# Kernel optimization log

Measured on AMD Instinct MI355X. Metric: run time of the kernel, lower is better.

## Reference

```python
import jax, jax.numpy as jnp
import numpy as np

NUM_HEADS = 16
NUM_KV_HEADS = 4
HEAD_DIM = 128
ROPE_DIMS = 64
EPS = 1.1920929e-07  # torch.finfo(float32).eps, used by F.rms_norm(eps=None)


def rms_norm(x):
    ms = jnp.mean(jnp.square(x), axis=-1, keepdims=True)
    return x * jax.lax.rsqrt(ms + EPS)


def apply_rotary(x, cos, sin):
    # x: [..., s, rope_dims]; cos/sin: [s, rope_dims//2]
    h = x.shape[-1] // 2
    x1, x2 = x[..., :h], x[..., h:]
    return jnp.concatenate([x1 * cos + x2 * sin, -x1 * sin + x2 * cos], axis=-1)


def setup_inputs() -> dict:
    key = jax.random.key(0)
    ks = jax.random.split(key, 5)
    b, s, d = 2, 2048, 2048
    return {
        "x": jax.random.normal(ks[0], (b, s, d), jnp.float32),
        "q_w": jax.random.normal(ks[1], (d, d), jnp.float32) * 0.02,
        "k_w": jax.random.normal(ks[2], (NUM_KV_HEADS * HEAD_DIM, d), jnp.float32) * 0.02,
        "v_w": jax.random.normal(ks[3], (NUM_KV_HEADS * HEAD_DIM, d), jnp.float32) * 0.02,
        "out_w": jax.random.normal(ks[4], (d, d), jnp.float32) * 0.02,
        "q_gain": jnp.full((NUM_HEADS,), 12.0, jnp.float32),
    }


def reference(x, q_w, k_w, v_w, out_w, q_gain):
    b, s, d = x.shape
    g = NUM_HEADS // NUM_KV_HEADS

    q = (x @ q_w.T).reshape(b, s, NUM_HEADS, HEAD_DIM).transpose(0, 2, 1, 3)
    k = (x @ k_w.T).reshape(b, s, NUM_KV_HEADS, HEAD_DIM).transpose(0, 2, 1, 3)
    v = (x @ v_w.T).reshape(b, s, NUM_KV_HEADS, HEAD_DIM).transpose(0, 2, 1, 3)

    q = rms_norm(q)
    k = rms_norm(k)

    # partial rotary embedding
    t = jnp.arange(s, dtype=jnp.float32)
    inv_freq = 1.0 / (10000.0 ** (jnp.arange(0, ROPE_DIMS, 2, dtype=jnp.float32) / ROPE_DIMS))
    f = jnp.outer(t, inv_freq)                      # [s, rope_dims//2]
    cos, sin = jnp.cos(f), jnp.sin(f)

    q = jnp.concatenate([apply_rotary(q[..., :ROPE_DIMS], cos, sin), q[..., ROPE_DIMS:]], axis=-1)
    q = q * q_gain[None, :, None, None]
    k = jnp.concatenate([apply_rotary(k[..., :ROPE_DIMS], cos, sin), k[..., ROPE_DIMS:]], axis=-1)

    # GQA-native causal attention (no repeated K/V materialization)
    qg = q.reshape(b, NUM_KV_HEADS, g, s, HEAD_DIM)
    scale = 1.0 / jnp.sqrt(jnp.float32(HEAD_DIM))
    scores = jnp.einsum("bkgqd,bkld->bkgql", qg, k) * scale
    causal = jnp.tril(jnp.ones((s, s), bool))
    scores = jnp.where(causal, scores, jnp.finfo(scores.dtype).min)
    p = jax.nn.softmax(scores, axis=-1)
    y = jnp.einsum("bkgql,bkld->bkgqd", p, v)       # [b, kvh, g, s, hd]
    y = y.reshape(b, NUM_HEADS, s, HEAD_DIM).transpose(0, 2, 1, 3).reshape(b, s, d)
    return y @ out_w.T
```

## Files before the change

### kernel.cpp

```cpp
#include <hip/hip_runtime.h>
#include <cmath>


#define S_LEN 2048
#define DMODEL 2048
#define NH 16
#define NKV 4
#define HD 128

#define NEG_SENT -1.0e30f
#define QK_SCALE 0.08838834764831845f

typedef _Float16 f16x8 __attribute__((ext_vector_type(8)));
typedef float f32x4 __attribute__((ext_vector_type(4)));

static __device__ __forceinline__ short f2h(float f) {
  _Float16 h = (_Float16)f;
  return *(short*)&h;
}
static __device__ __forceinline__ float h2f(short s) {
  _Float16 h = *(_Float16*)&s;
  return (float)h;
}

static __device__ __forceinline__ void stage16(const short* g, short* ldsbase) {
  __builtin_amdgcn_global_load_lds(
      (const __attribute__((address_space(1))) void*)g,
      (__attribute__((address_space(3))) void*)ldsbase, 16, 0, 0);
}

__global__ __launch_bounds__(256) void f32_to_f16(const float* __restrict__ src,
                                                  short* __restrict__ dst, int n) {
  int i = (blockIdx.x * 256 + threadIdx.x) * 4;
  if (i < n) {
    float4 v = *reinterpret_cast<const float4*>(src + i);
    short4 o;
    o.x = f2h(v.x); o.y = f2h(v.y); o.z = f2h(v.z); o.w = f2h(v.w);
    *reinterpret_cast<short4*>(dst + i) = o;
  }
}

template <bool F32OUT>
static __device__ __forceinline__ void gemm_core(const short* __restrict__ A,
                                                 const short* __restrict__ W,
                                                 void* __restrict__ Cv,
                                                 int N, int K, int bm, int bn) {
  __shared__ __align__(16) short As[128][64];
  __shared__ __align__(16) short Ws[128][64];
  const int tid = threadIdx.x;
  const int wave = tid >> 6, lane = tid & 63;
  const int quad = lane >> 4, l16 = lane & 15;
  const int wm = (wave >> 1) * 64, wn = (wave & 1) * 64;

  f32x4 acc[4][4];
#pragma unroll
  for (int i = 0; i < 4; i++)
#pragma unroll
    for (int j = 0; j < 4; j++) acc[i][j] = f32x4{0.f, 0.f, 0.f, 0.f};

  const int srow = wave * 8 + (lane >> 3);
  const int scol = (lane & 7) * 8;

  for (int k0 = 0; k0 < K; k0 += 64) {
    __syncthreads();
#pragma unroll
    for (int i = 0; i < 4; i++) {
      stage16(A + (size_t)(bm + srow + i * 32) * K + k0 + scol,
              &As[wave * 8 + i * 32][0]);
      stage16(W + (size_t)(bn + srow + i * 32) * K + k0 + scol,
              &Ws[wave * 8 + i * 32][0]);
    }
    __syncthreads();
#pragma unroll
    for (int kk = 0; kk < 64; kk += 32) {
      f16x8 af[4], bfr[4];
#pragma unroll
      for (int mi = 0; mi < 4; mi++)
        af[mi] = *reinterpret_cast<const f16x8*>(&As[wm + mi * 16 + l16][kk + quad * 8]);
#pragma unroll
      for (int ni = 0; ni < 4; ni++)
        bfr[ni] = *reinterpret_cast<const f16x8*>(&Ws[wn + ni * 16 + l16][kk + quad * 8]);
#pragma unroll
      for (int mi = 0; mi < 4; mi++)
#pragma unroll
        for (int ni = 0; ni < 4; ni++)
          acc[mi][ni] = __builtin_amdgcn_mfma_f32_16x16x32_f16(af[mi], bfr[ni], acc[mi][ni], 0, 0, 0);
    }
  }
#pragma unroll
  for (int mi = 0; mi < 4; mi++)
#pragma unroll
    for (int ni = 0; ni < 4; ni++) {
      int gr = bm + wm + mi * 16 + quad * 4;
      int gc = bn + wn + ni * 16 + l16;
#pragma unroll
      for (int r = 0; r < 4; r++) {
        if (F32OUT)
          ((float*)Cv)[(size_t)(gr + r) * N + gc] = acc[mi][ni][r];
        else
          ((short*)Cv)[(size_t)(gr + r) * N + gc] = f2h(acc[mi][ni][r]);
      }
    }
}

template <bool F32OUT>
__global__ __launch_bounds__(256) void gemm_bt(const short* __restrict__ A,
                                               const short* __restrict__ W,
                                               void* __restrict__ Cv,
                                               int N, int K) {
  gemm_core<F32OUT>(A, W, Cv, N, K, blockIdx.x * 128, blockIdx.y * 128);
}

__global__ __launch_bounds__(256) void gemm_kv(const short* __restrict__ A,
                                               const short* __restrict__ W0,
                                               const short* __restrict__ W1,
                                               short* __restrict__ C0,
                                               short* __restrict__ C1,
                                               int N, int K) {
  const short* W = blockIdx.z ? W1 : W0;
  short* C = blockIdx.z ? C1 : C0;
  gemm_core<false>(A, W, (void*)C, N, K, blockIdx.x * 128, blockIdx.y * 128);
}

__global__ __launch_bounds__(256) void postproc(const short* __restrict__ src,
                                                short* __restrict__ dst,
                                                const float* __restrict__ gain,
                                                int n_heads, int mode) {
  int gw = blockIdx.x * 4 + (threadIdx.x >> 6);
  int lane = threadIdx.x & 63;
  int head = gw % n_heads;
  int token = gw / n_heads;
  int s = token & (S_LEN - 1);
  int b = token >> 11;
  const short* sp = src + (size_t)token * (n_heads * HD) + head * HD;
  float v0 = h2f(sp[lane]);
  float v1 = h2f(sp[lane + 64]);
  float ss = v0 * v0 + v1 * v1;
#pragma unroll
  for (int off = 1; off < 64; off <<= 1) ss += __shfl_xor(ss, off, 64);
  float sc = rsqrtf(ss * (1.0f / 128.0f) + 1.1920929e-07f);
  v0 *= sc;
  v1 *= sc;
  int i = lane & 31;
  float inv = powf(10000.0f, -((float)(2 * i) * (1.0f / 64.0f)));
  float f = (float)s * inv;
  float cs, sn;
  sincosf(f, &sn, &cs);
  float partner = __shfl_xor(v0, 32, 64);
  v0 = (lane < 32) ? (v0 * cs + partner * sn) : (v0 * cs - partner * sn);
  if (mode == 2) {
    float g = gain[head] * QK_SCALE;
    v0 *= g;
    v1 *= g;
  }
  short* dp = dst + ((size_t)(b * n_heads + head) * S_LEN + s) * HD;
  dp[lane] = f2h(v0);
  dp[lane + 64] = f2h(v1);
}

__global__ __launch_bounds__(256) void v_transpose(const short* __restrict__ src,
                                                   short* __restrict__ dst) {
  __shared__ __align__(16) short t[64][72];
  const int tid = threadIdx.x;
  const int s0 = blockIdx.x * 64;
  const int d0 = blockIdx.y * 64;
#pragma unroll
  for (int i = 0; i < 2; i++) {
    int r = (tid >> 3) + i * 32;
    int c = (tid & 7) * 8;
    *reinterpret_cast<int4*>(&t[r][c]) =
        *reinterpret_cast<const int4*>(src + (size_t)(s0 + r) * 512 + d0 + c);
  }
  __syncthreads();
  const int b = s0 >> 11;
  const int sbase = s0 & (S_LEN - 1);
#pragma unroll
  for (int i = 0; i < 2; i++) {
    int dr = (tid >> 3) + i * 32;
    int sc8 = (tid & 7) * 8;
    int d = d0 + dr;
    int kv = d >> 7, dw = d & 127;
    short4 lo, hi;
    lo.x = t[sc8 + 0][dr]; lo.y = t[sc8 + 1][dr];
    lo.z = t[sc8 + 2][dr]; lo.w = t[sc8 + 3][dr];
    hi.x = t[sc8 + 4][dr]; hi.y = t[sc8 + 5][dr];
    hi.z = t[sc8 + 6][dr]; hi.w = t[sc8 + 7][dr];
    short* dp = dst + (((size_t)(b * NKV + kv) * HD + dw) * S_LEN) + sbase + sc8;
    *reinterpret_cast<short4*>(dp) = lo;
    *reinterpret_cast<short4*>(dp + 4) = hi;
  }
}

__global__ __launch_bounds__(256, 2) void attn_fwd(const short* __restrict__ qb,
                                                   const short* __restrict__ kb,
                                                   const short* __restrict__ vT,
                                                   short* __restrict__ out) {
  __shared__ __align__(16) short k_lds[64][136];
  __shared__ __align__(16) short vt_lds[144][72];
  __shared__ __align__(16) short p_lds[4][16][136];

  const int tid = threadIdx.x, wave = tid >> 6, lane = tid & 63;
  const int quad = lane >> 4, l16 = lane & 15;
  const int bh = blockIdx.y;
  const int b = bh >> 4, h = bh & 15;
  const int kvh = h >> 2;
  const int pj = blockIdx.x;

  const short* kptr = kb + ((size_t)(b * NKV + kvh) * S_LEN) * HD;
  const short* vtp  = vT + ((size_t)(b * NKV + kvh) * HD) * S_LEN;

  const int kr = (tid >> 4), kc = (tid & 15) * 8;
  const int vr = (tid >> 3), vc = (tid & 7) * 8;

  {
    int r = 128 + (tid >> 4);
    int c = (tid & 15) * 4;
    short val = (r == 128) ? (short)0x3C00 : (short)0;
    short4 v4 = {val, val, val, val};
    *reinterpret_cast<short4*>(&vt_lds[r][c]) = v4;
  }

  for (int pass = 0; pass < 2; pass++) {
    const int qsub = pass ? (31 - pj) : pj;
    const int q0 = qsub * 64 + wave * 16;
    const short* qptr = qb + ((size_t)(b * NH + h) * S_LEN + q0) * HD;

    f16x8 qf[4];
#pragma unroll
    for (int st = 0; st < 4; st++)
      qf[st] = *reinterpret_cast<const f16x8*>(
          qptr + (size_t)l16 * HD + st * 32 + quad * 8);

    f32x4 o[9];
#pragma unroll
    for (int i = 0; i < 9; i++) o[i] = f32x4{0.f, 0.f, 0.f, 0.f};
    float m_i[4] = {NEG_SENT, NEG_SENT, NEG_SENT, NEG_SENT};

    const int ktiles = qsub + 1;
    for (int kt = 0; kt < ktiles; kt++) {
      const int kbase = kt * 64;
      __syncthreads();
#pragma unroll
      for (int i = 0; i < 4; i++)
        *reinterpret_cast<int4*>(&k_lds[kr + i * 16][kc]) =
            *reinterpret_cast<const int4*>(kptr + (size_t)(kbase + kr + i * 16) * HD + kc);
#pragma unroll
      for (int i = 0; i < 4; i++)
        *reinterpret_cast<int4*>(&vt_lds[vr + i * 32][vc]) =
            *reinterpret_cast<const int4*>(vtp + (size_t)(vr + i * 32) * S_LEN + kbase + vc);
      __syncthreads();

      f32x4 sc[4];
#pragma unroll
      for (int ct = 0; ct < 4; ct++) sc[ct] = f32x4{0.f, 0.f, 0.f, 0.f};
#pragma unroll
      for (int ct = 0; ct < 4; ct++) {
#pragma unroll
        for (int st = 0; st < 4; st++) {
          f16x8 kf = *reinterpret_cast<const f16x8*>(&k_lds[ct * 16 + l16][st * 32 + quad * 8]);
          sc[ct] = __builtin_amdgcn_mfma_f32_16x16x32_f16(qf[st], kf, sc[ct], 0, 0, 0);
        }
      }

      if (kbase + 63 > q0) {
#pragma unroll
        for (int ct = 0; ct < 4; ct++)
#pragma unroll
          for (int r = 0; r < 4; r++) {
            int qrow = q0 + quad * 4 + r;
            int col = kbase + ct * 16 + l16;
            sc[ct][r] = (col <= qrow) ? sc[ct][r] : NEG_SENT;
          }
      }

      float cand[4];
#pragma unroll
      for (int r = 0; r < 4; r++)
        cand[r] = fmaxf(fmaxf(sc[0][r], sc[1][r]), fmaxf(sc[2][r], sc[3][r]));
#pragma unroll
      for (int off = 1; off < 16; off <<= 1)
#pragma unroll
        for (int r = 0; r < 4; r++)
          cand[r] = fmaxf(cand[r], __shfl_xor(cand[r], off, 64));

      bool ch = (cand[0] > m_i[0]) | (cand[1] > m_i[1]) |
                (cand[2] > m_i[2]) | (cand[3] > m_i[3]);
      if (__any(ch)) {
        float alpha[4];
#pragma unroll
        for (int r = 0; r < 4; r++) {
          float mn = fmaxf(m_i[r], cand[r]);
          alpha[r] = __expf(m_i[r] - mn);
          m_i[r] = mn;
        }
#pragma unroll
        for (int nt = 0; nt < 9; nt++)
#pragma unroll
          for (int r = 0; r < 4; r++) o[nt][r] *= alpha[r];
      }

#pragma unroll
      for (int ct = 0; ct < 4; ct++)
#pragma unroll
        for (int r = 0; r < 4; r++) {
          float p = __expf(sc[ct][r] - m_i[r]);
          p_lds[wave][quad * 4 + r][ct * 16 + l16] = f2h(p);
        }

      f16x8 pf0 = *reinterpret_cast<const f16x8*>(&p_lds[wave][l16][quad * 8]);
      f16x8 pf1 = *reinterpret_cast<const f16x8*>(&p_lds[wave][l16][32 + quad * 8]);
#pragma unroll
      for (int nt = 0; nt < 9; nt++) {
        f16x8 vf0 = *reinterpret_cast<const f16x8*>(&vt_lds[nt * 16 + l16][quad * 8]);
        f16x8 vf1 = *reinterpret_cast<const f16x8*>(&vt_lds[nt * 16 + l16][32 + quad * 8]);
        o[nt] = __builtin_amdgcn_mfma_f32_16x16x32_f16(pf0, vf0, o[nt], 0, 0, 0);
        o[nt] = __builtin_amdgcn_mfma_f32_16x16x32_f16(pf1, vf1, o[nt], 0, 0, 0);
      }
    }

    float inv_l[4];
#pragma unroll
    for (int r = 0; r < 4; r++) {
      float l = __shfl(o[8][r], lane & 48, 64);
      inv_l[r] = 1.0f / fmaxf(l, 1e-20f);
    }
#pragma unroll
    for (int nt = 0; nt < 8; nt++)
#pragma unroll
      for (int r = 0; r < 4; r++) {
        int srow = q0 + quad * 4 + r;
        int dcol = nt * 16 + l16;
        out[((size_t)(b * S_LEN + srow)) * DMODEL + h * HD + dcol] =
            f2h(o[nt][r] * inv_l[r]);
      }
  }
}

extern "C" void kernel_launch(void* const* d_in, const int* in_sizes, int n_in,
                              void* d_out, int out_size, void* d_ws, size_t ws_size,
                              hipStream_t stream) {
  const float* x      = (const float*)d_in[0];
  const float* q_w    = (const float*)d_in[1];
  const float* k_w    = (const float*)d_in[2];
  const float* v_w    = (const float*)d_in[3];
  const float* out_w  = (const float*)d_in[4];
  const float* q_gain = (const float*)d_in[5];
  float* out = (float*)d_out;

  const int BS = 2 * S_LEN;
  short* xb   = (short*)d_ws;
  short* wqb  = xb   + (size_t)8 * 1024 * 1024;
  short* wkb  = wqb  + (size_t)4 * 1024 * 1024;
  short* wvb  = wkb  + (size_t)1 * 1024 * 1024;
  short* wob  = wvb  + (size_t)1 * 1024 * 1024;
  short* qraw = wob  + (size_t)4 * 1024 * 1024;
  short* kraw = qraw + (size_t)8 * 1024 * 1024;
  short* vraw = kraw + (size_t)2 * 1024 * 1024;
  short* qbuf = vraw + (size_t)2 * 1024 * 1024;
  short* kbuf = qbuf + (size_t)8 * 1024 * 1024;
  short* vT   = kbuf + (size_t)2 * 1024 * 1024;
  short* attn = qraw;

  dim3 blk(256);
  f32_to_f16<<<8192, blk, 0, stream>>>(x, xb, BS * DMODEL);
  f32_to_f16<<<4096, blk, 0, stream>>>(q_w, wqb, DMODEL * DMODEL);
  f32_to_f16<<<1024, blk, 0, stream>>>(k_w, wkb, 512 * DMODEL);
  f32_to_f16<<<1024, blk, 0, stream>>>(v_w, wvb, 512 * DMODEL);
  f32_to_f16<<<4096, blk, 0, stream>>>(out_w, wob, DMODEL * DMODEL);

  gemm_bt<false><<<dim3(32, 16), blk, 0, stream>>>(xb, wqb, qraw, 2048, 2048);
  gemm_kv<<<dim3(32, 4, 2), blk, 0, stream>>>(xb, wkb, wvb, kraw, vraw, 512, 2048);

  postproc<<<dim3((BS * NH) / 4), blk, 0, stream>>>(qraw, qbuf, q_gain, NH, 2);
  postproc<<<dim3((BS * NKV) / 4), blk, 0, stream>>>(kraw, kbuf, q_gain, NKV, 1);
  v_transpose<<<dim3(BS / 64, 8), blk, 0, stream>>>(vraw, vT);

  attn_fwd<<<dim3(16, 2 * NH), blk, 0, stream>>>(qbuf, kbuf, vT, attn);

  gemm_bt<true><<<dim3(32, 16), blk, 0, stream>>>(attn, wob, out, 2048, 2048);
}
```

Baseline: 387.7 us.

## Fuse fp32-to-fp16 casts, prefetch K/V tiles in registers, remap attention grid

Merges the five conversion launches into one kernel that picks its source buffer by global index. In attention, the next K/V tile is loaded into registers while the current tile is computed, so global latency overlaps with MFMA work. The launch becomes a 1D grid ordered so blocks sharing a KV head run close together, which should help L2 reuse. p_lds is also shrunk, freeing LDS, at the cost of extra register pressure from the prefetch buffers.

```diff
diff --git a/kernel.cpp b/kernel.cpp
--- a/kernel.cpp
+++ b/kernel.cpp
@@ -29,15 +29,31 @@
       (__attribute__((address_space(3))) void*)ldsbase, 16, 0, 0);
 }
 
-__global__ __launch_bounds__(256) void f32_to_f16(const float* __restrict__ src,
-                                                  short* __restrict__ dst, int n) {
-  int i = (blockIdx.x * 256 + threadIdx.x) * 4;
-  if (i < n) {
-    float4 v = *reinterpret_cast<const float4*>(src + i);
-    short4 o;
-    o.x = f2h(v.x); o.y = f2h(v.y); o.z = f2h(v.z); o.w = f2h(v.w);
-    *reinterpret_cast<short4*>(dst + i) = o;
-  }
+__global__ __launch_bounds__(256) void f32_to_f16_all(
+    const float* __restrict__ s0, const float* __restrict__ s1,
+    const float* __restrict__ s2, const float* __restrict__ s3,
+    const float* __restrict__ s4, short* __restrict__ d0,
+    short* __restrict__ d1, short* __restrict__ d2, short* __restrict__ d3,
+    short* __restrict__ d4) {
+  int u = blockIdx.x * 256 + threadIdx.x;
+  const float* src;
+  short* dst;
+  int off;
+  if (u < 2097152) {
+    src = s0; dst = d0; off = u;
+  } else if (u < 3145728) {
+    src = s1; dst = d1; off = u - 2097152;
+  } else if (u < 3407872) {
+    src = s2; dst = d2; off = u - 3145728;
+  } else if (u < 3670016) {
+    src = s3; dst = d3; off = u - 3407872;
+  } else {
+    src = s4; dst = d4; off = u - 3670016;
+  }
+  float4 v = *reinterpret_cast<const float4*>(src + (size_t)off * 4);
+  short4 o;
+  o.x = f2h(v.x); o.y = f2h(v.y); o.z = f2h(v.z); o.w = f2h(v.w);
+  *reinterpret_cast<short4*>(dst + (size_t)off * 4) = o;
 }
 
 template <bool F32OUT>
@@ -197,14 +213,17 @@
                                                    short* __restrict__ out) {
   __shared__ __align__(16) short k_lds[64][136];
   __shared__ __align__(16) short vt_lds[144][72];
-  __shared__ __align__(16) short p_lds[4][16][136];
+  __shared__ __align__(16) short p_lds[4][16][72];
 
   const int tid = threadIdx.x, wave = tid >> 6, lane = tid & 63;
   const int quad = lane >> 4, l16 = lane & 15;
-  const int bh = blockIdx.y;
-  const int b = bh >> 4, h = bh & 15;
-  const int kvh = h >> 2;
-  const int pj = blockIdx.x;
+  const int D = blockIdx.x;
+  const int strm = D & 7;
+  const int t = D >> 3;
+  const int pj = t >> 2;
+  const int b = strm >> 2;
+  const int kvh = strm & 3;
+  const int h = kvh * 4 + (t & 3);
 
   const short* kptr = kb + ((size_t)(b * NKV + kvh) * S_LEN) * HD;
   const short* vtp  = vT + ((size_t)(b * NKV + kvh) * HD) * S_LEN;
@@ -237,18 +256,35 @@
     float m_i[4] = {NEG_SENT, NEG_SENT, NEG_SENT, NEG_SENT};
 
     const int ktiles = qsub + 1;
+
+    int4 gk[4], gv[4];
+#pragma unroll
+    for (int i = 0; i < 4; i++)
+      gk[i] = *reinterpret_cast<const int4*>(kptr + (size_t)(kr + i * 16) * HD + kc);
+#pragma unroll
+    for (int i = 0; i < 4; i++)
+      gv[i] = *reinterpret_cast<const int4*>(vtp + (size_t)(vr + i * 32) * S_LEN + vc);
+
     for (int kt = 0; kt < ktiles; kt++) {
       const int kbase = kt * 64;
       __syncthreads();
 #pragma unroll
       for (int i = 0; i < 4; i++)
-        *reinterpret_cast<int4*>(&k_lds[kr + i * 16][kc]) =
-            *reinterpret_cast<const int4*>(kptr + (size_t)(kbase + kr + i * 16) * HD + kc);
+        *reinterpret_cast<int4*>(&k_lds[kr + i * 16][kc]) = gk[i];
 #pragma unroll
       for (int i = 0; i < 4; i++)
-        *reinterpret_cast<int4*>(&vt_lds[vr + i * 32][vc]) =
-            *reinterpret_cast<const int4*>(vtp + (size_t)(vr + i * 32) * S_LEN + kbase + vc);
+        *reinterpret_cast<int4*>(&vt_lds[vr + i * 32][vc]) = gv[i];
       __syncthreads();
+
+      if (kt + 1 < ktiles) {
+        const int nb = kbase + 64;
+#pragma unroll
+        for (int i = 0; i < 4; i++)
+          gk[i] = *reinterpret_cast<const int4*>(kptr + (size_t)(nb + kr + i * 16) * HD + kc);
+#pragma unroll
+        for (int i = 0; i < 4; i++)
+          gv[i] = *reinterpret_cast<const int4*>(vtp + (size_t)(vr + i * 32) * S_LEN + nb + vc);
+      }
 
       f32x4 sc[4];
 #pragma unroll
@@ -362,11 +398,8 @@
   short* attn = qraw;
 
   dim3 blk(256);
-  f32_to_f16<<<8192, blk, 0, stream>>>(x, xb, BS * DMODEL);
-  f32_to_f16<<<4096, blk, 0, stream>>>(q_w, wqb, DMODEL * DMODEL);
-  f32_to_f16<<<1024, blk, 0, stream>>>(k_w, wkb, 512 * DMODEL);
-  f32_to_f16<<<1024, blk, 0, stream>>>(v_w, wvb, 512 * DMODEL);
-  f32_to_f16<<<4096, blk, 0, stream>>>(out_w, wob, DMODEL * DMODEL);
+  f32_to_f16_all<<<18432, blk, 0, stream>>>(x, q_w, k_w, v_w, out_w,
+                                            xb, wqb, wkb, wvb, wob);
 
   gemm_bt<false><<<dim3(32, 16), blk, 0, stream>>>(xb, wqb, qraw, 2048, 2048);
   gemm_kv<<<dim3(32, 4, 2), blk, 0, stream>>>(xb, wkb, wvb, kraw, vraw, 512, 2048);
@@ -375,7 +408,7 @@
   postproc<<<dim3((BS * NKV) / 4), blk, 0, stream>>>(kraw, kbuf, q_gain, NKV, 1);
   v_transpose<<<dim3(BS / 64, 8), blk, 0, stream>>>(vraw, vT);
 
-  attn_fwd<<<dim3(16, 2 * NH), blk, 0, stream>>>(qbuf, kbuf, vT, attn);
+  attn_fwd<<<dim3(512), blk, 0, stream>>>(qbuf, kbuf, vT, attn);
 
   gemm_bt<true><<<dim3(32, 16), blk, 0, stream>>>(attn, wob, out, 2048, 2048);
 }
```

New measurement: 462.8 us. 1.19x slower.
